# Optimization experiments

Measured on AMD Instinct MI355X. Metric: run time of the kernel, lower is better.

The kernel has to match this reference:

```python
import jax, jax.numpy as jnp
import numpy as np
import math

B, S, D, H, FF, L, V = 4, 2048, 512, 8, 2048, 4, 256
WINDOW, STRIDE, NGLOBAL = 256, 128, 16  # sparse pattern: causal & (local | strided | global)


def setup_inputs() -> dict:
    key = jax.random.key(0)
    ks = jax.random.split(key, 12)
    g = lambda k, shp: jax.random.normal(k, shp, dtype=jnp.float32) * 0.02
    return {
        "src_tokens": jax.random.randint(ks[0], (B, S), 0, V, dtype=jnp.int32),
        "emb": g(ks[1], (V, D)),
        "b_out": jnp.zeros((V,), jnp.float32),
        "Wq": g(ks[2], (L, D, D)), "bq": jnp.zeros((L, D), jnp.float32),
        "Wk": g(ks[3], (L, D, D)), "bk": jnp.zeros((L, D), jnp.float32),
        "Wv": g(ks[4], (L, D, D)), "bv": jnp.zeros((L, D), jnp.float32),
        "Wo": g(ks[5], (L, D, D)), "bo": jnp.zeros((L, D), jnp.float32),
        "ln1_g": jnp.ones((L, D), jnp.float32), "ln1_b": jnp.zeros((L, D), jnp.float32),
        "W1": g(ks[6], (L, D, FF)), "b1": jnp.zeros((L, FF), jnp.float32),
        "W2": g(ks[7], (L, FF, D)), "b2": jnp.zeros((L, D), jnp.float32),
        "ln2_g": jnp.ones((L, D), jnp.float32), "ln2_b": jnp.zeros((L, D), jnp.float32),
    }


def _pos_enc(seq_len, d_model):
    pos = jnp.arange(seq_len, dtype=jnp.float32)[:, None]
    div = jnp.exp(jnp.arange(0, d_model, 2, dtype=jnp.float32) * (-math.log(10000.0) / d_model))
    pe = jnp.zeros((seq_len, d_model), jnp.float32)
    pe = pe.at[:, 0::2].set(jnp.sin(pos * div)).at[:, 1::2].set(jnp.cos(pos * div))
    return pe


def _ln(x, g, b):
    m = x.mean(-1, keepdims=True)
    v = ((x - m) ** 2).mean(-1, keepdims=True)
    return (x - m) * jax.lax.rsqrt(v + 1e-5) * g + b


def _sparse_mask(seq_len):
    i = jnp.arange(seq_len)[:, None]
    j = jnp.arange(seq_len)[None, :]
    causal = j <= i
    local = (i - j) < WINDOW
    strided = ((i - j) % STRIDE) == 0
    glob = j < NGLOBAL
    return causal & (local | strided | glob)  # [S, S] bool


def reference(src_tokens, emb, b_out, Wq, bq, Wk, bk, Wv, bv, Wo, bo,
              ln1_g, ln1_b, W1, b1, W2, b2, ln2_g, ln2_b):
    dh = D // H
    x = emb[src_tokens] * math.sqrt(D) + _pos_enc(S, D)  # [B,S,D] (dropout inactive at eval)
    mask = _sparse_mask(S)
    for l in range(L):
        q = (x @ Wq[l] + bq[l]).reshape(B, S, H, dh)
        k = (x @ Wk[l] + bk[l]).reshape(B, S, H, dh)
        v = (x @ Wv[l] + bv[l]).reshape(B, S, H, dh)
        scores = jnp.einsum('bihd,bjhd->bhij', q, k) / math.sqrt(dh)
        scores = jnp.where(mask, scores, jnp.float32(-1e9))
        attn = jax.nn.softmax(scores, axis=-1)
        o = jnp.einsum('bhij,bjhd->bihd', attn, v).reshape(B, S, D)
        x = _ln(x + o @ Wo[l] + bo[l], ln1_g[l], ln1_b[l])      # post-LN residual
        h = jax.nn.relu(x @ W1[l] + b1[l])
        x = _ln(x + h @ W2[l] + b2[l], ln2_g[l], ln2_b[l])
    return x @ emb.T + b_out  # tied output projection -> [B,S,V]
```

## Files before the change

### kernel.cpp

```cpp
#include <hip/hip_runtime.h>
#include <hip/hip_bf16.h>
#include <math.h>

#define B_  4
#define S_  2048
#define D_  512
#define H_  8
#define DH_ 64
#define FF_ 2048
#define L_  4
#define V_  256
#define NTOK (B_ * S_)
#define XN  ((size_t)NTOK * D_)

typedef __attribute__((ext_vector_type(8))) short bf16x8;
typedef __attribute__((ext_vector_type(4))) float f32x4;
typedef __attribute__((ext_vector_type(8))) unsigned short u16x8;
typedef __attribute__((ext_vector_type(4))) unsigned short u16x4;

typedef const __attribute__((address_space(1))) unsigned int* gptr_u32;
typedef __attribute__((address_space(3))) unsigned int* lptr_u32;

__device__ __forceinline__ float bf2f(unsigned short u) {
    return __uint_as_float((unsigned)u << 16);
}
__device__ __forceinline__ unsigned short f2bf_bits(float f) {
    __hip_bfloat16 t = __float2bfloat16(f);
    return *(unsigned short*)&t;
}

__global__ void pe_table_kernel(float* __restrict__ PE) {
    int s = blockIdx.x;
    int d = threadIdx.x * 2;
    float ang = (float)s * expf((float)d * (-logf(10000.0f) / (float)D_));
    PE[(size_t)s * D_ + d]     = sinf(ang);
    PE[(size_t)s * D_ + d + 1] = cosf(ang);
}

__global__ void embed_kernel(const int* __restrict__ tok,
                             const float* __restrict__ emb,
                             const float* __restrict__ PE,
                             float* __restrict__ X,
                             __hip_bfloat16* __restrict__ Xb) {
    int bs = blockIdx.x;
    int s = bs % S_;
    int t = tok[bs];
    const float scale = 22.62741699796952f;
    int d = threadIdx.x * 4;
    float4 e = *(const float4*)(emb + (size_t)t * D_ + d);
    float4 p = *(const float4*)(PE + (size_t)s * D_ + d);
    float4 v = make_float4(e.x * scale + p.x, e.y * scale + p.y,
                           e.z * scale + p.z, e.w * scale + p.w);
    *(float4*)(X + (size_t)bs * D_ + d) = v;
    u16x4 pk = { f2bf_bits(v.x), f2bf_bits(v.y), f2bf_bits(v.z), f2bf_bits(v.w) };
    *(u16x4*)((unsigned short*)Xb + (size_t)bs * D_ + d) = pk;
}

__global__ void transpose_conv_kernel(const float* __restrict__ W,
                                      __hip_bfloat16* __restrict__ Wt,
                                      int K, int N) {
    const float* Wl = W + (size_t)blockIdx.z * K * N;
    __hip_bfloat16* Wtl = Wt + (size_t)blockIdx.z * K * N;
    __shared__ float t[32][33];
    int k0 = blockIdx.y * 32, n0 = blockIdx.x * 32;
    int tx = threadIdx.x & 31, ty = threadIdx.x >> 5;
    #pragma unroll
    for (int q = 0; q < 4; ++q)
        t[ty + q * 8][tx] = Wl[(size_t)(k0 + ty + q * 8) * N + n0 + tx];
    __syncthreads();
    #pragma unroll
    for (int q = 0; q < 4; ++q)
        Wtl[(size_t)(n0 + ty + q * 8) * K + k0 + tx] =
            __float2bfloat16(t[tx][ty + q * 8]);
}

__global__ void transpose_qkv_kernel(const float* __restrict__ Wq,
                                     const float* __restrict__ Wk,
                                     const float* __restrict__ Wv,
                                     __hip_bfloat16* __restrict__ dst) {
    int z = blockIdx.z, l = z / 3, which = z % 3;
    const float* src = (which == 0 ? Wq : which == 1 ? Wk : Wv) + (size_t)l * D_ * D_;
    __hip_bfloat16* d = dst + (size_t)l * 1536 * D_ + (size_t)which * D_ * D_;
    __shared__ float t[32][33];
    int k0 = blockIdx.y * 32, n0 = blockIdx.x * 32;
    int tx = threadIdx.x & 31, ty = threadIdx.x >> 5;
    #pragma unroll
    for (int q = 0; q < 4; ++q)
        t[ty + q * 8][tx] = src[(size_t)(k0 + ty + q * 8) * D_ + n0 + tx];
    __syncthreads();
    #pragma unroll
    for (int q = 0; q < 4; ++q)
        d[(size_t)(n0 + ty + q * 8) * D_ + k0 + tx] =
            __float2bfloat16(t[tx][ty + q * 8]);
}

__global__ void conv_bf16_kernel(const float* __restrict__ in,
                                 __hip_bfloat16* __restrict__ out, int n) {
    int i = blockIdx.x * 256 + threadIdx.x;
    if (i < n) out[i] = __float2bfloat16(in[i]);
}

template <int BM, int RELU, int OUT_MODE>
__global__ __launch_bounds__(256)
void gemm_bf16_kernel(const __hip_bfloat16* __restrict__ A,
                      const __hip_bfloat16* __restrict__ Bt,
                      const float* __restrict__ bias0,
                      const float* __restrict__ bias1,
                      const float* __restrict__ bias2,
                      float* __restrict__ Cf,
                      __hip_bfloat16* __restrict__ Cb0,
                      __hip_bfloat16* __restrict__ Cb1,
                      __hip_bfloat16* __restrict__ Cb2,
                      __hip_bfloat16* __restrict__ CbT,
                      int M, int N, int K) {
    constexpr int MI = BM / 32;
    __shared__ unsigned short As[2][BM * 32];
    __shared__ unsigned short Bs[2][128 * 32];
    int tid = threadIdx.x;
    int lane = tid & 63, wid = tid >> 6;
    int wm = (wid >> 1) * (BM / 2), wn = (wid & 1) * 64;
    int g = lane >> 4, il = lane & 15;

    int gx = gridDim.x;
    int fid = blockIdx.x + gx * blockIdx.y;
    int cpx = (gx * gridDim.y) >> 3;
    int swz = (fid & 7) * cpx + (fid >> 3);
    int m0 = (swz / gx) * BM, n0 = (swz % gx) * 128;

    auto stage = [&](int buf, int k0) {
        #pragma unroll
        for (int q = 0; q < BM / 64; ++q) {
            int idx = q * 256 + tid;
            int r = idx >> 2, c = idx & 3;
            int csw = (c ^ r) & 3;
            const __hip_bfloat16* sa = A + (size_t)(m0 + r) * K + k0 + csw * 8;
            __builtin_amdgcn_global_load_lds((gptr_u32)(const void*)sa,
                                             (lptr_u32)(void*)&As[buf][idx * 8], 16, 0, 0);
        }
        #pragma unroll
        for (int q = 0; q < 2; ++q) {
            int idx = q * 256 + tid;
            int r = idx >> 2, c = idx & 3;
            int csw = (c ^ r) & 3;
            const __hip_bfloat16* sb = Bt + (size_t)(n0 + r) * K + k0 + csw * 8;
            __builtin_amdgcn_global_load_lds((gptr_u32)(const void*)sb,
                                             (lptr_u32)(void*)&Bs[buf][idx * 8], 16, 0, 0);
        }
    };

    f32x4 acc[MI][4] = {};
    int NT = K >> 5;
    stage(0, 0);

    for (int t = 0; t < NT; ++t) {
        int cur = t & 1;
        if (t + 1 < NT) {
            stage(cur ^ 1, (t + 1) << 5);
            if constexpr (BM == 128)
                asm volatile("s_waitcnt vmcnt(4)" ::: "memory");
            else
                asm volatile("s_waitcnt vmcnt(3)" ::: "memory");
        } else {
            asm volatile("s_waitcnt vmcnt(0)" ::: "memory");
        }
        __builtin_amdgcn_s_barrier();

        bf16x8 af[MI], bf[4];
        #pragma unroll
        for (int i = 0; i < MI; ++i) {
            int m = wm + i * 16 + il;
            af[i] = *(const bf16x8*)&As[cur][m * 32 + ((g ^ m) & 3) * 8];
        }
        #pragma unroll
        for (int j = 0; j < 4; ++j) {
            int n = wn + j * 16 + il;
            bf[j] = *(const bf16x8*)&Bs[cur][n * 32 + ((g ^ n) & 3) * 8];
        }
        #pragma unroll
        for (int i = 0; i < MI; ++i)
            #pragma unroll
            for (int j = 0; j < 4; ++j)
                acc[i][j] = __builtin_amdgcn_mfma_f32_16x16x32_bf16(
                    af[i], bf[j], acc[i][j], 0, 0, 0);

        __builtin_amdgcn_s_barrier();
    }

    if constexpr (OUT_MODE == 4) {
        int seg = n0 >> 9;
        const float* bias = seg == 0 ? bias0 : seg == 1 ? bias1 : bias2;
        __hip_bfloat16* Crow = seg == 0 ? Cb0 : seg == 1 ? Cb1 : Cb2;
        int nseg = n0 & 511;
        #pragma unroll
        for (int j = 0; j < 4; ++j) {
            int coll = nseg + wn + j * 16 + il;
            float bv = bias[coll];
            #pragma unroll
            for (int i = 0; i < MI; ++i) {
                int row0 = m0 + wm + i * 16 + g * 4;
                if (seg < 2) {
                    #pragma unroll
                    for (int r = 0; r < 4; ++r)
                        Crow[(size_t)(row0 + r) * 512 + coll] =
                            __float2bfloat16(acc[i][j][r] + bv);
                } else {
                    u16x4 pk;
                    #pragma unroll
                    for (int r = 0; r < 4; ++r) {
                        float v = acc[i][j][r] + bv;
                        Crow[(size_t)(row0 + r) * 512 + coll] = __float2bfloat16(v);
                        pk[r] = f2bf_bits(v);
                    }
                    int hh = coll >> 6, dh = coll & 63;
                    int bb = row0 >> 11, s0 = row0 & 2047;
                    *(u16x4*)(CbT + ((size_t)((bb * 8 + hh) * 64 + dh) * 2048 + s0)) = pk;
                }
            }
        }
    } else {
        #pragma unroll
        for (int j = 0; j < 4; ++j) {
            int col = n0 + wn + j * 16 + il;
            float bv = bias0[col];
            #pragma unroll
            for (int i = 0; i < MI; ++i) {
                #pragma unroll
                for (int r = 0; r < 4; ++r) {
                    int row = m0 + wm + i * 16 + g * 4 + r;
                    float v = acc[i][j][r] + bv;
                    if (RELU) v = fmaxf(v, 0.0f);
                    if (OUT_MODE == 1) Cb0[(size_t)row * N + col] = __float2bfloat16(v);
                    else               Cf[(size_t)row * N + col] = v;
                }
            }
        }
    }
}

__device__ __forceinline__ bf16x8 lds_frag(const unsigned short* base, int row, int chunk) {
    int byte = (row << 7) + (((chunk ^ (row & 7)) & 7) << 4);
    return *(const bf16x8*)((const char*)base + byte);
}

__global__ __launch_bounds__(256)
void attn_mfma_kernel(const __hip_bfloat16* __restrict__ Q,
                      const __hip_bfloat16* __restrict__ K,
                      const __hip_bfloat16* __restrict__ V,
                      const __hip_bfloat16* __restrict__ VT,
                      __hip_bfloat16* __restrict__ O) {
    __shared__ unsigned short Ks[2][64 * 64];
    __shared__ unsigned short Vs[2][64 * 64];
    __shared__ unsigned short Ps[4][16 * 64];

    int fid = blockIdx.x + 32 * (blockIdx.y + 8 * blockIdx.z);
    int swz = (fid & 7) * 128 + (fid >> 3);
    int i0 = (swz & 31) * 64;
    int h  = (swz >> 5) & 7;
    int b  = swz >> 8;

    int tid = threadIdx.x, lane = tid & 63, wv = tid >> 6;
    int g = lane >> 4, il = lane & 15, g4 = g * 4;

    int nloc = min(i0 >> 6, 4) + 1;
    int add0 = (i0 > 256);
    int nt = nloc + add0;

    const size_t vt_off = (size_t)((b * 8 + h) * 64) * 2048;
    auto j0_of = [&](int t) { return (t < nloc) ? (i0 - 64 * t) : 0; };

    auto stage = [&](int buf, int j0) {
        #pragma unroll
        for (int q = 0; q < 2; ++q) {
            int idx = q * 256 + tid;
            int row = idx >> 3, c = idx & 7;
            int csw = c ^ (row & 7);
            const __hip_bfloat16* sk = K + (size_t)(b * 2048 + j0 + row) * 512 + h * 64 + csw * 8;
            __builtin_amdgcn_global_load_lds((gptr_u32)(const void*)sk,
                                             (lptr_u32)(void*)&Ks[buf][idx * 8], 16, 0, 0);
            const __hip_bfloat16* sv = VT + vt_off + (size_t)row * 2048 + j0 + csw * 8;
            __builtin_amdgcn_global_load_lds((gptr_u32)(const void*)sv,
                                             (lptr_u32)(void*)&Vs[buf][idx * 8], 16, 0, 0);
        }
    };

    int iq = i0 + wv * 16 + il;
    bf16x8 qf[2];
    #pragma unroll
    for (int kh = 0; kh < 2; ++kh)
        qf[kh] = *(const bf16x8*)(Q + (size_t)(b * 2048 + iq) * 512 + h * 64 + kh * 32 + g * 8);

    stage(0, j0_of(0));

    float qfl[16];
    #pragma unroll
    for (int kh = 0; kh < 2; ++kh)
        #pragma unroll
        for (int e = 0; e < 8; ++e)
            qfl[kh * 8 + e] = bf2f(((u16x8)qf[kh])[e]);

    unsigned short* myP = Ps[wv];
    f32x4 o[4] = {};
    float os[16] = {};
    float m = -1e30f, l = 0.0f;
    const float CSC = 0.18033688011112042f;

    const unsigned short* Kbase = (const unsigned short*)(K + (size_t)b * 2048 * 512 + h * 64);
    const unsigned short* Vbase = (const unsigned short*)(V + (size_t)b * 2048 * 512 + h * 64);
    for (int j = iq - 384; j >= 16; j -= 128) {
        const unsigned short* kr = Kbase + (size_t)j * 512;
        u16x8 k0 = *(const u16x8*)(kr + g * 8);
        u16x8 k1 = *(const u16x8*)(kr + 32 + g * 8);
        float dot = 0.0f;
        #pragma unroll
        for (int e = 0; e < 8; ++e)
            dot += qfl[e] * bf2f(k0[e]) + qfl[8 + e] * bf2f(k1[e]);
        dot += __shfl_xor(dot, 16);
        dot += __shfl_xor(dot, 32);
        float s2 = dot * CSC;
        float mn = fmaxf(m, s2);
        float al = exp2f(m - mn);
        float p = exp2f(s2 - mn);
        l = l * al + p;
        m = mn;
        const unsigned short* vr = Vbase + (size_t)j * 512;
        u16x8 v0 = *(const u16x8*)(vr + g * 8);
        u16x8 v1 = *(const u16x8*)(vr + 32 + g * 8);
        #pragma unroll
        for (int e = 0; e < 8; ++e) {
            os[e]     = os[e]     * al + p * bf2f(v0[e]);
            os[8 + e] = os[8 + e] * al + p * bf2f(v1[e]);
        }
    }

    for (int t = 0; t < nt; ++t) {
        __syncthreads();
        int cur = t & 1;
        if (t + 1 < nt) stage(cur ^ 1, j0_of(t + 1));
        int j0 = j0_of(t);
        bool gtile = (t >= nloc);
        bool dtile = (t == 0);

        f32x4 s[4] = {};
        __builtin_amdgcn_s_setprio(1);
        if (gtile) {
            #pragma unroll
            for (int kh = 0; kh < 2; ++kh) {
                bf16x8 a = lds_frag(Ks[cur], il, kh * 4 + g);
                s[0] = __builtin_amdgcn_mfma_f32_16x16x32_bf16(a, qf[kh], s[0], 0, 0, 0);
            }
        } else if (dtile) {
            #pragma unroll
            for (int kh = 0; kh < 2; ++kh)
                #pragma unroll
                for (int jn = 0; jn < 4; ++jn)
                    if (jn <= wv) {
                        bf16x8 a = lds_frag(Ks[cur], jn * 16 + il, kh * 4 + g);
                        s[jn] = __builtin_amdgcn_mfma_f32_16x16x32_bf16(a, qf[kh], s[jn], 0, 0, 0);
                    }
        } else {
            #pragma unroll
            for (int kh = 0; kh < 2; ++kh)
                #pragma unroll
                for (int jn = 0; jn < 4; ++jn) {
                    bf16x8 a = lds_frag(Ks[cur], jn * 16 + il, kh * 4 + g);
                    s[jn] = __builtin_amdgcn_mfma_f32_16x16x32_bf16(a, qf[kh], s[jn], 0, 0, 0);
                }
        }
        __builtin_amdgcn_s_setprio(0);

        float mloc = -1e30f;
        if (gtile) {
            #pragma unroll
            for (int r = 0; r < 4; ++r) {
                float sv = s[0][r] * CSC;
                s[0][r] = sv;
                mloc = fmaxf(mloc, sv);
            }
        } else if (dtile) {
            #pragma unroll
            for (int jn = 0; jn < 4; ++jn) {
                if (jn < wv) {
                    #pragma unroll
                    for (int r = 0; r < 4; ++r) {
                        float sv = s[jn][r] * CSC;
                        s[jn][r] = sv;
                        mloc = fmaxf(mloc, sv);
                    }
                } else if (jn == wv) {
                    #pragma unroll
                    for (int r = 0; r < 4; ++r) {
                        float sv = (g4 + r <= il) ? s[jn][r] * CSC : -1e30f;
                        s[jn][r] = sv;
                        mloc = fmaxf(mloc, sv);
                    }
                }
            }
        } else if (t == 4) {
            #pragma unroll
            for (int jn = 0; jn < 4; ++jn)
                #pragma unroll
                for (int r = 0; r < 4; ++r) {
                    int jg = j0 + jn * 16 + g4 + r;
                    int dij = iq - jg;
                    bool ok = (dij < 256) || ((dij & 127) == 0) || (jg < 16);
                    float sv = ok ? s[jn][r] * CSC : -1e30f;
                    s[jn][r] = sv;
                    mloc = fmaxf(mloc, sv);
                }
        } else {
            #pragma unroll
            for (int jn = 0; jn < 4; ++jn)
                #pragma unroll
                for (int r = 0; r < 4; ++r) {
                    float sv = s[jn][r] * CSC;
                    s[jn][r] = sv;
                    mloc = fmaxf(mloc, sv);
                }
        }
        mloc = fmaxf(mloc, __shfl_xor(mloc, 16));
        mloc = fmaxf(mloc, __shfl_xor(mloc, 32));
        float mn = fmaxf(m, mloc);
        float al = exp2f(m - mn);

        float lloc = 0.0f;
        if (gtile) {
            #pragma unroll
            for (int r = 0; r < 4; ++r) {
                float p = exp2f(s[0][r] - mn);
                s[0][r] = p;
                lloc += p;
            }
        } else {
            #pragma unroll
            for (int jn = 0; jn < 4; ++jn) {
                if (dtile && jn > wv) continue;
                #pragma unroll
                for (int r = 0; r < 4; ++r) {
                    float p = exp2f(s[jn][r] - mn);
                    s[jn][r] = p;
                    lloc += p;
                }
            }
        }
        lloc += __shfl_xor(lloc, 16);
        lloc += __shfl_xor(lloc, 32);
        l = l * al + lloc;
        m = mn;

        if (!__all(al == 1.0f)) {
            float ar[4];
            #pragma unroll
            for (int r = 0; r < 4; ++r) ar[r] = __shfl(al, g4 + r);
            #pragma unroll
            for (int dn = 0; dn < 4; ++dn)
                #pragma unroll
                for (int r = 0; r < 4; ++r) o[dn][r] *= ar[r];
            #pragma unroll
            for (int e = 0; e < 16; ++e) os[e] *= al;
        }

        #pragma unroll
        for (int jn = 0; jn < 4; ++jn) {
            if (gtile && jn >= 2) continue;
            u16x4 pk = { 0, 0, 0, 0 };
            bool live = gtile ? (jn == 0) : (!dtile || jn <= wv);
            if (live) {
                #pragma unroll
                for (int r = 0; r < 4; ++r) pk[r] = f2bf_bits(s[jn][r]);
            }
            int byte = ((il << 7) + (jn << 5) + (g << 3)) ^ ((il & 7) << 4);
            *(u16x4*)((char*)myP + byte) = pk;
        }
        int khmax = (gtile || (dtile && wv < 2)) ? 1 : 2;
        __builtin_amdgcn_s_setprio(1);
        #pragma unroll
        for (int kh = 0; kh < 2; ++kh) {
            if (kh < khmax) {
                bf16x8 pa = lds_frag(myP, il, kh * 4 + g);
                #pragma unroll
                for (int dn = 0; dn < 4; ++dn) {
                    bf16x8 bv = lds_frag(Vs[cur], dn * 16 + il, kh * 4 + g);
                    o[dn] = __builtin_amdgcn_mfma_f32_16x16x32_bf16(pa, bv, o[dn], 0, 0, 0);
                }
            }
        }
        __builtin_amdgcn_s_setprio(0);
    }

    __syncthreads();
    float* osl = (float*)&Ks[0][0] + wv * 1024;
    #pragma unroll
    for (int kh = 0; kh < 2; ++kh)
        #pragma unroll
        for (int e = 0; e < 8; ++e)
            osl[il * 64 + kh * 32 + g * 8 + e] = os[kh * 8 + e];
    __syncthreads();

    float li[4];
    #pragma unroll
    for (int r = 0; r < 4; ++r) li[r] = 1.0f / __shfl(l, g4 + r);
    #pragma unroll
    for (int dn = 0; dn < 4; ++dn)
        #pragma unroll
        for (int r = 0; r < 4; ++r) {
            int row = i0 + wv * 16 + g4 + r;
            float add = osl[(g4 + r) * 64 + dn * 16 + il];
            O[(size_t)(b * 2048 + row) * 512 + h * 64 + dn * 16 + il] =
                __float2bfloat16((o[dn][r] + add) * li[r]);
        }
}

__global__ __launch_bounds__(256)
void add_ln_kernel(float* __restrict__ X,
                   const __hip_bfloat16* __restrict__ T,
                   const float* __restrict__ g,
                   const float* __restrict__ bb,
                   __hip_bfloat16* __restrict__ Xb) {
    size_t row = blockIdx.x * 4 + (threadIdx.x >> 6);
    int lane = threadIdx.x & 63;
    int d0 = lane * 8;
    float4 x0 = *(const float4*)(X + row * D_ + d0);
    float4 x1 = *(const float4*)(X + row * D_ + d0 + 4);
    u16x8 tv = *(const u16x8*)((const unsigned short*)T + row * D_ + d0);
    float v[8] = { x0.x + bf2f(tv[0]), x0.y + bf2f(tv[1]),
                   x0.z + bf2f(tv[2]), x0.w + bf2f(tv[3]),
                   x1.x + bf2f(tv[4]), x1.y + bf2f(tv[5]),
                   x1.z + bf2f(tv[6]), x1.w + bf2f(tv[7]) };
    float sum = 0.0f;
    #pragma unroll
    for (int q = 0; q < 8; ++q) sum += v[q];
    #pragma unroll
    for (int o = 32; o; o >>= 1) sum += __shfl_xor(sum, o);
    float mean = sum * (1.0f / D_);
    float var = 0.0f;
    #pragma unroll
    for (int q = 0; q < 8; ++q) { float dd = v[q] - mean; var += dd * dd; }
    #pragma unroll
    for (int o = 32; o; o >>= 1) var += __shfl_xor(var, o);
    var *= (1.0f / D_);
    float r = rsqrtf(var + 1e-5f);
    float4 g0 = *(const float4*)(g + d0),  g1 = *(const float4*)(g + d0 + 4);
    float4 b0 = *(const float4*)(bb + d0), b1 = *(const float4*)(bb + d0 + 4);
    float y[8];
    y[0] = (v[0]-mean)*r*g0.x+b0.x; y[1] = (v[1]-mean)*r*g0.y+b0.y;
    y[2] = (v[2]-mean)*r*g0.z+b0.z; y[3] = (v[3]-mean)*r*g0.w+b0.w;
    y[4] = (v[4]-mean)*r*g1.x+b1.x; y[5] = (v[5]-mean)*r*g1.y+b1.y;
    y[6] = (v[6]-mean)*r*g1.z+b1.z; y[7] = (v[7]-mean)*r*g1.w+b1.w;
    *(float4*)(X + row * D_ + d0)     = make_float4(y[0], y[1], y[2], y[3]);
    *(float4*)(X + row * D_ + d0 + 4) = make_float4(y[4], y[5], y[6], y[7]);
    u16x8 pk;
    #pragma unroll
    for (int q = 0; q < 8; ++q) pk[q] = f2bf_bits(y[q]);
    *(u16x8*)((unsigned short*)Xb + row * D_ + d0) = pk;
}

extern "C" void kernel_launch(void* const* d_in, const int* in_sizes, int n_in,
                              void* d_out, int out_size, void* d_ws, size_t ws_size,
                              hipStream_t stream) {
    const int*   tok   = (const int*)  d_in[0];
    const float* emb   = (const float*)d_in[1];
    const float* b_out = (const float*)d_in[2];
    const float* Wq    = (const float*)d_in[3];
    const float* bq    = (const float*)d_in[4];
    const float* Wk    = (const float*)d_in[5];
    const float* bk    = (const float*)d_in[6];
    const float* Wv    = (const float*)d_in[7];
    const float* bv    = (const float*)d_in[8];
    const float* Wo    = (const float*)d_in[9];
    const float* bo    = (const float*)d_in[10];
    const float* ln1g  = (const float*)d_in[11];
    const float* ln1b  = (const float*)d_in[12];
    const float* W1    = (const float*)d_in[13];
    const float* b1    = (const float*)d_in[14];
    const float* W2    = (const float*)d_in[15];
    const float* b2    = (const float*)d_in[16];
    const float* ln2g  = (const float*)d_in[17];
    const float* ln2b  = (const float*)d_in[18];
    float* out = (float*)d_out;

    char* w = (char*)d_ws;
    auto alloc = [&](size_t bytes) {
        char* p = w;
        w += (bytes + 255) & ~(size_t)255;
        return p;
    };
    float*          X   = (float*)         alloc(XN * 4);
    __hip_bfloat16* Xb  = (__hip_bfloat16*)alloc(XN * 2);
    __hip_bfloat16* Tb  = (__hip_bfloat16*)alloc(XN * 2);
    char* uni = alloc(XN * 2 * 5);
    __hip_bfloat16* Qb  = (__hip_bfloat16*)uni;
    __hip_bfloat16* Kb  = Qb + XN;
    __hip_bfloat16* Vb  = Kb + XN;
    __hip_bfloat16* VTb = Vb + XN;
    __hip_bfloat16* Ob  = VTb + XN;
    __hip_bfloat16* Hb  = (__hip_bfloat16*)uni;
    __hip_bfloat16* Wqkvt = (__hip_bfloat16*)alloc((size_t)L_ * 1536 * D_ * 2);
    __hip_bfloat16* Wot  = (__hip_bfloat16*)alloc((size_t)L_ * D_ * D_ * 2);
    __hip_bfloat16* W1t  = (__hip_bfloat16*)alloc((size_t)L_ * D_ * FF_ * 2);
    __hip_bfloat16* W2t  = (__hip_bfloat16*)alloc((size_t)L_ * FF_ * D_ * 2);
    __hip_bfloat16* embb = (__hip_bfloat16*)alloc((size_t)V_ * D_ * 2);
    float*          PE   = (float*)alloc((size_t)S_ * D_ * 4);

    {
        pe_table_kernel<<<S_, 256, 0, stream>>>(PE);
        dim3 gqkv(D_ / 32, D_ / 32, L_ * 3);
        transpose_qkv_kernel<<<gqkv, 256, 0, stream>>>(Wq, Wk, Wv, Wqkvt);
        dim3 gdd(D_ / 32, D_ / 32, L_);
        transpose_conv_kernel<<<gdd, 256, 0, stream>>>(Wo, Wot, D_, D_);
        dim3 g1(FF_ / 32, D_ / 32, L_);
        transpose_conv_kernel<<<g1, 256, 0, stream>>>(W1, W1t, D_, FF_);
        dim3 g2(D_ / 32, FF_ / 32, L_);
        transpose_conv_kernel<<<g2, 256, 0, stream>>>(W2, W2t, FF_, D_);
        conv_bf16_kernel<<<(V_ * D_ + 255) / 256, 256, 0, stream>>>(emb, embb, V_ * D_);
    }

    embed_kernel<<<NTOK, 128, 0, stream>>>(tok, emb, PE, X, Xb);

    dim3 blk(256);
    dim3 gqkv(1536 / 128, NTOK / 128);
    dim3 g512n(D_ / 128, NTOK / 64);
    dim3 gff (FF_ / 128, NTOK / 128);
    dim3 gout(V_ / 128, NTOK / 64);
    dim3 gattn(S_ / 64, H_, B_);
    dim3 gln(NTOK / 4);

    for (int l = 0; l < L_; ++l) {
        const __hip_bfloat16* wqkv = Wqkvt + (size_t)l * 1536 * D_;
        const __hip_bfloat16* wot = Wot + (size_t)l * D_ * D_;
        const __hip_bfloat16* w1t = W1t + (size_t)l * D_ * FF_;
        const __hip_bfloat16* w2t = W2t + (size_t)l * FF_ * D_;

        gemm_bf16_kernel<128, 0, 4><<<gqkv, blk, 0, stream>>>(
            Xb, wqkv, bq + l * D_, bk + l * D_, bv + l * D_,
            nullptr, Qb, Kb, Vb, VTb, NTOK, 1536, D_);

        attn_mfma_kernel<<<gattn, blk, 0, stream>>>(Qb, Kb, Vb, VTb, Ob);

        gemm_bf16_kernel<64, 0, 1><<<g512n, blk, 0, stream>>>(
            Ob, wot, bo + l * D_, nullptr, nullptr,
            nullptr, Tb, nullptr, nullptr, nullptr, NTOK, D_, D_);
        add_ln_kernel<<<gln, blk, 0, stream>>>(X, Tb, ln1g + l * D_, ln1b + l * D_, Xb);

        gemm_bf16_kernel<128, 1, 1><<<gff, blk, 0, stream>>>(
            Xb, w1t, b1 + l * FF_, nullptr, nullptr,
            nullptr, Hb, nullptr, nullptr, nullptr, NTOK, FF_, D_);
        gemm_bf16_kernel<64, 0, 1><<<g512n, blk, 0, stream>>>(
            Hb, w2t, b2 + l * D_, nullptr, nullptr,
            nullptr, Tb, nullptr, nullptr, nullptr, NTOK, D_, FF_);
        add_ln_kernel<<<gln, blk, 0, stream>>>(X, Tb, ln2g + l * D_, ln2b + l * D_, Xb);
    }

    gemm_bf16_kernel<64, 0, 0><<<gout, blk, 0, stream>>>(
        Xb, embb, b_out, nullptr, nullptr,
        out, nullptr, nullptr, nullptr, nullptr, NTOK, V_, D_);
}
```

Before: 692.5 us.

## Pair complementary query tiles per attention block and batch strided-key softmax

```diff
diff --git a/kernel.cpp b/kernel.cpp
--- a/kernel.cpp
+++ b/kernel.cpp
@@ -252,21 +252,20 @@
     __shared__ unsigned short Vs[2][64 * 64];
     __shared__ unsigned short Ps[4][16 * 64];
 
-    int fid = blockIdx.x + 32 * (blockIdx.y + 8 * blockIdx.z);
-    int swz = (fid & 7) * 128 + (fid >> 3);
-    int i0 = (swz & 31) * 64;
-    int h  = (swz >> 5) & 7;
-    int b  = swz >> 8;
+    int d = blockIdx.x + 16 * (blockIdx.y + 8 * blockIdx.z);
+    int xcd = d & 7, t8 = d >> 3;
+    int qtr = t8 & 15, gsub = t8 >> 4;
+    int qt = ((qtr & 1) << 3) | ((qtr & 2) << 1) | ((qtr & 4) >> 1) | ((qtr & 8) >> 3);
+    int grp = xcd * 4 + gsub;
+    int h = grp & 7, b = grp >> 3;
 
     int tid = threadIdx.x, lane = tid & 63, wv = tid >> 6;
     int g = lane >> 4, il = lane & 15, g4 = g * 4;
 
-    int nloc = min(i0 >> 6, 4) + 1;
-    int add0 = (i0 > 256);
-    int nt = nloc + add0;
-
     const size_t vt_off = (size_t)((b * 8 + h) * 64) * 2048;
-    auto j0_of = [&](int t) { return (t < nloc) ? (i0 - 64 * t) : 0; };
+    const unsigned short* Kbase = (const unsigned short*)(K + (size_t)b * 2048 * 512 + h * 64);
+    const unsigned short* Vbase = (const unsigned short*)(V + (size_t)b * 2048 * 512 + h * 64);
+    const float CSC = 0.18033688011112042f;
 
     auto stage = [&](int buf, int j0) {
         #pragma unroll
@@ -283,231 +282,257 @@
         }
     };
 
-    int iq = i0 + wv * 16 + il;
-    bf16x8 qf[2];
-    #pragma unroll
-    for (int kh = 0; kh < 2; ++kh)
-        qf[kh] = *(const bf16x8*)(Q + (size_t)(b * 2048 + iq) * 512 + h * 64 + kh * 32 + g * 8);
-
-    stage(0, j0_of(0));
-
-    float qfl[16];
-    #pragma unroll
-    for (int kh = 0; kh < 2; ++kh)
-        #pragma unroll
-        for (int e = 0; e < 8; ++e)
-            qfl[kh * 8 + e] = bf2f(((u16x8)qf[kh])[e]);
-
     unsigned short* myP = Ps[wv];
-    f32x4 o[4] = {};
-    float os[16] = {};
-    float m = -1e30f, l = 0.0f;
-    const float CSC = 0.18033688011112042f;
-
-    const unsigned short* Kbase = (const unsigned short*)(K + (size_t)b * 2048 * 512 + h * 64);
-    const unsigned short* Vbase = (const unsigned short*)(V + (size_t)b * 2048 * 512 + h * 64);
-    for (int j = iq - 384; j >= 16; j -= 128) {
-        const unsigned short* kr = Kbase + (size_t)j * 512;
-        u16x8 k0 = *(const u16x8*)(kr + g * 8);
-        u16x8 k1 = *(const u16x8*)(kr + 32 + g * 8);
-        float dot = 0.0f;
-        #pragma unroll
-        for (int e = 0; e < 8; ++e)
-            dot += qfl[e] * bf2f(k0[e]) + qfl[8 + e] * bf2f(k1[e]);
-        dot += __shfl_xor(dot, 16);
-        dot += __shfl_xor(dot, 32);
-        float s2 = dot * CSC;
-        float mn = fmaxf(m, s2);
-        float al = exp2f(m - mn);
-        float p = exp2f(s2 - mn);
-        l = l * al + p;
-        m = mn;
-        const unsigned short* vr = Vbase + (size_t)j * 512;
-        u16x8 v0 = *(const u16x8*)(vr + g * 8);
-        u16x8 v1 = *(const u16x8*)(vr + 32 + g * 8);
-        #pragma unroll
-        for (int e = 0; e < 8; ++e) {
-            os[e]     = os[e]     * al + p * bf2f(v0[e]);
-            os[8 + e] = os[8 + e] * al + p * bf2f(v1[e]);
-        }
-    }
-
-    for (int t = 0; t < nt; ++t) {
+
+    #pragma unroll 1
+    for (int half = 0; half < 2; ++half) {
+        int i0 = (half == 0) ? qt * 64 : (31 - qt) * 64;
+        int nloc = min(i0 >> 6, 4) + 1;
+        int add0 = (i0 > 256);
+        int nt = nloc + add0;
+        auto j0_of = [&](int t) { return (t < nloc) ? (i0 - 64 * t) : 0; };
+
         __syncthreads();
-        int cur = t & 1;
-        if (t + 1 < nt) stage(cur ^ 1, j0_of(t + 1));
-        int j0 = j0_of(t);
-        bool gtile = (t >= nloc);
-        bool dtile = (t == 0);
-
-        f32x4 s[4] = {};
-        __builtin_amdgcn_s_setprio(1);
-        if (gtile) {
-            #pragma unroll
-            for (int kh = 0; kh < 2; ++kh) {
-                bf16x8 a = lds_frag(Ks[cur], il, kh * 4 + g);
-                s[0] = __builtin_amdgcn_mfma_f32_16x16x32_bf16(a, qf[kh], s[0], 0, 0, 0);
-            }
-        } else if (dtile) {
-            #pragma unroll
-            for (int kh = 0; kh < 2; ++kh)
-                #pragma unroll
-                for (int jn = 0; jn < 4; ++jn)
-                    if (jn <= wv) {
+        stage(0, i0);
+
+        int iq = i0 + wv * 16 + il;
+        bf16x8 qf[2];
+        #pragma unroll
+        for (int kh = 0; kh < 2; ++kh)
+            qf[kh] = *(const bf16x8*)(Q + (size_t)(b * 2048 + iq) * 512 + h * 64 + kh * 32 + g * 8);
+        float qfl[16];
+        #pragma unroll
+        for (int kh = 0; kh < 2; ++kh)
+            #pragma unroll
+            for (int e = 0; e < 8; ++e)
+                qfl[kh * 8 + e] = bf2f(((u16x8)qf[kh])[e]);
+
+        f32x4 o[4] = {};
+        float os[16] = {};
+        float m = -1e30f, l = 0.0f;
+
+        int nst = (iq >= 400) ? ((iq - 400) >> 7) + 1 : 0;
+        if (nst > 0) {
+            float sarr[13];
+            #pragma unroll
+            for (int mm = 0; mm < 13; ++mm) {
+                int j = iq - 384 - 128 * mm;
+                int jc = (j >= 16) ? j : 16;
+                const unsigned short* kr = Kbase + (size_t)jc * 512;
+                u16x8 k0 = *(const u16x8*)(kr + g * 8);
+                u16x8 k1 = *(const u16x8*)(kr + 32 + g * 8);
+                float dot = 0.0f;
+                #pragma unroll
+                for (int e = 0; e < 8; ++e)
+                    dot += qfl[e] * bf2f(k0[e]) + qfl[8 + e] * bf2f(k1[e]);
+                dot += __shfl_xor(dot, 16);
+                dot += __shfl_xor(dot, 32);
+                sarr[mm] = (j >= 16) ? dot * CSC : -1e30f;
+            }
+            float mmax = -1e30f;
+            #pragma unroll
+            for (int mm = 0; mm < 13; ++mm) mmax = fmaxf(mmax, sarr[mm]);
+            float p[13];
+            float lsum = 0.0f;
+            #pragma unroll
+            for (int mm = 0; mm < 13; ++mm) {
+                p[mm] = exp2f(sarr[mm] - mmax);
+                lsum += p[mm];
+            }
+            #pragma unroll
+            for (int mm = 0; mm < 13; ++mm) {
+                int j = iq - 384 - 128 * mm;
+                int jc = (j >= 16) ? j : 16;
+                const unsigned short* vr = Vbase + (size_t)jc * 512;
+                u16x8 v0 = *(const u16x8*)(vr + g * 8);
+                u16x8 v1 = *(const u16x8*)(vr + 32 + g * 8);
+                #pragma unroll
+                for (int e = 0; e < 8; ++e) {
+                    os[e]     += p[mm] * bf2f(v0[e]);
+                    os[8 + e] += p[mm] * bf2f(v1[e]);
+                }
+            }
+            m = mmax;
+            l = lsum;
+        }
+
+        for (int t = 0; t < nt; ++t) {
+            __syncthreads();
+            int cur = t & 1;
+            if (t + 1 < nt) stage(cur ^ 1, j0_of(t + 1));
+            int j0 = j0_of(t);
+            bool gtile = (t >= nloc);
+            bool dtile = (t == 0);
+
+            f32x4 s[4] = {};
+            __builtin_amdgcn_s_setprio(1);
+            if (gtile) {
+                #pragma unroll
+                for (int kh = 0; kh < 2; ++kh) {
+                    bf16x8 a = lds_frag(Ks[cur], il, kh * 4 + g);
+                    s[0] = __builtin_amdgcn_mfma_f32_16x16x32_bf16(a, qf[kh], s[0], 0, 0, 0);
+                }
+            } else if (dtile) {
+                #pragma unroll
+                for (int kh = 0; kh < 2; ++kh)
+                    #pragma unroll
+                    for (int jn = 0; jn < 4; ++jn)
+                        if (jn <= wv) {
+                            bf16x8 a = lds_frag(Ks[cur], jn * 16 + il, kh * 4 + g);
+                            s[jn] = __builtin_amdgcn_mfma_f32_16x16x32_bf16(a, qf[kh], s[jn], 0, 0, 0);
+                        }
+            } else {
+                #pragma unroll
+                for (int kh = 0; kh < 2; ++kh)
+                    #pragma unroll
+                    for (int jn = 0; jn < 4; ++jn) {
                         bf16x8 a = lds_frag(Ks[cur], jn * 16 + il, kh * 4 + g);
                         s[jn] = __builtin_amdgcn_mfma_f32_16x16x32_bf16(a, qf[kh], s[jn], 0, 0, 0);
                     }
-        } else {
-            #pragma unroll
-            for (int kh = 0; kh < 2; ++kh)
+            }
+            __builtin_amdgcn_s_setprio(0);
+
+            float mloc = -1e30f;
+            if (gtile) {
+                #pragma unroll
+                for (int r = 0; r < 4; ++r) {
+                    float sv = s[0][r] * CSC;
+                    s[0][r] = sv;
+                    mloc = fmaxf(mloc, sv);
+                }
+            } else if (dtile) {
                 #pragma unroll
                 for (int jn = 0; jn < 4; ++jn) {
-                    bf16x8 a = lds_frag(Ks[cur], jn * 16 + il, kh * 4 + g);
-                    s[jn] = __builtin_amdgcn_mfma_f32_16x16x32_bf16(a, qf[kh], s[jn], 0, 0, 0);
-                }
-        }
-        __builtin_amdgcn_s_setprio(0);
-
-        float mloc = -1e30f;
-        if (gtile) {
-            #pragma unroll
-            for (int r = 0; r < 4; ++r) {
-                float sv = s[0][r] * CSC;
-                s[0][r] = sv;
-                mloc = fmaxf(mloc, sv);
-            }
-        } else if (dtile) {
-            #pragma unroll
-            for (int jn = 0; jn < 4; ++jn) {
-                if (jn < wv) {
+                    if (jn < wv) {
+                        #pragma unroll
+                        for (int r = 0; r < 4; ++r) {
+                            float sv = s[jn][r] * CSC;
+                            s[jn][r] = sv;
+                            mloc = fmaxf(mloc, sv);
+                        }
+                    } else if (jn == wv) {
+                        #pragma unroll
+                        for (int r = 0; r < 4; ++r) {
+                            float sv = (g4 + r <= il) ? s[jn][r] * CSC : -1e30f;
+                            s[jn][r] = sv;
+                            mloc = fmaxf(mloc, sv);
+                        }
+                    }
+                }
+            } else if (t == 4) {
+                #pragma unroll
+                for (int jn = 0; jn < 4; ++jn)
+                    #pragma unroll
+                    for (int r = 0; r < 4; ++r) {
+                        int jg = j0 + jn * 16 + g4 + r;
+                        int dij = iq - jg;
+                        bool ok = (dij < 256) || ((dij & 127) == 0) || (jg < 16);
+                        float sv = ok ? s[jn][r] * CSC : -1e30f;
+                        s[jn][r] = sv;
+                        mloc = fmaxf(mloc, sv);
+                    }
+            } else {
+                #pragma unroll
+                for (int jn = 0; jn < 4; ++jn)
                     #pragma unroll
                     for (int r = 0; r < 4; ++r) {
                         float sv = s[jn][r] * CSC;
                         s[jn][r] = sv;
                         mloc = fmaxf(mloc, sv);
                     }
-                } else if (jn == wv) {
+            }
+            mloc = fmaxf(mloc, __shfl_xor(mloc, 16));
+            mloc = fmaxf(mloc, __shfl_xor(mloc, 32));
+            float mn = fmaxf(m, mloc);
+            float al = exp2f(m - mn);
+
+            float lloc = 0.0f;
+            if (gtile) {
+                #pragma unroll
+                for (int r = 0; r < 4; ++r) {
+                    float p = exp2f(s[0][r] - mn);
+                    s[0][r] = p;
+                    lloc += p;
+                }
+            } else {
+                #pragma unroll
+                for (int jn = 0; jn < 4; ++jn) {
+                    if (dtile && jn > wv) continue;
                     #pragma unroll
                     for (int r = 0; r < 4; ++r) {
-                        float sv = (g4 + r <= il) ? s[jn][r] * CSC : -1e30f;
-                        s[jn][r] = sv;
-                        mloc = fmaxf(mloc, sv);
+                        float p = exp2f(s[jn][r] - mn);
+                        s[jn][r] = p;
+                        lloc += p;
                     }
                 }
             }
-        } else if (t == 4) {
-            #pragma unroll
-            for (int jn = 0; jn < 4; ++jn)
-                #pragma unroll
-                for (int r = 0; r < 4; ++r) {
-                    int jg = j0 + jn * 16 + g4 + r;
-                    int dij = iq - jg;
-                    bool ok = (dij < 256) || ((dij & 127) == 0) || (jg < 16);
-                    float sv = ok ? s[jn][r] * CSC : -1e30f;
-                    s[jn][r] = sv;
-                    mloc = fmaxf(mloc, sv);
-                }
-        } else {
-            #pragma unroll
-            for (int jn = 0; jn < 4; ++jn)
-                #pragma unroll
-                for (int r = 0; r < 4; ++r) {
-                    float sv = s[jn][r] * CSC;
-                    s[jn][r] = sv;
-                    mloc = fmaxf(mloc, sv);
-                }
-        }
-        mloc = fmaxf(mloc, __shfl_xor(mloc, 16));
-        mloc = fmaxf(mloc, __shfl_xor(mloc, 32));
-        float mn = fmaxf(m, mloc);
-        float al = exp2f(m - mn);
-
-        float lloc = 0.0f;
-        if (gtile) {
+            lloc += __shfl_xor(lloc, 16);
+            lloc += __shfl_xor(lloc, 32);
+            l = l * al + lloc;
+            m = mn;
+
+            if (!__all(al == 1.0f)) {
+                float ar[4];
+                #pragma unroll
+                for (int r = 0; r < 4; ++r) ar[r] = __shfl(al, g4 + r);
+                #pragma unroll
+                for (int dn = 0; dn < 4; ++dn)
+                    #pragma unroll
+                    for (int r = 0; r < 4; ++r) o[dn][r] *= ar[r];
+                #pragma unroll
+                for (int e = 0; e < 16; ++e) os[e] *= al;
+            }
+
+            #pragma unroll
+            for (int jn = 0; jn < 4; ++jn) {
+                if (gtile && jn >= 2) continue;
+                u16x4 pk = { 0, 0, 0, 0 };
+                bool live = gtile ? (jn == 0) : (!dtile || jn <= wv);
+                if (live) {
+                    #pragma unroll
+                    for (int r = 0; r < 4; ++r) pk[r] = f2bf_bits(s[jn][r]);
+                }
+                int byte = ((il << 7) + (jn << 5) + (g << 3)) ^ ((il & 7) << 4);
+                *(u16x4*)((char*)myP + byte) = pk;
+            }
+            int khmax = (gtile || (dtile && wv < 2)) ? 1 : 2;
+            __builtin_amdgcn_s_setprio(1);
+            #pragma unroll
+            for (int kh = 0; kh < 2; ++kh) {
+                if (kh < khmax) {
+                    bf16x8 pa = lds_frag(myP, il, kh * 4 + g);
+                    #pragma unroll
+                    for (int dn = 0; dn < 4; ++dn) {
+                        bf16x8 bv = lds_frag(Vs[cur], dn * 16 + il, kh * 4 + g);
+                        o[dn] = __builtin_amdgcn_mfma_f32_16x16x32_bf16(pa, bv, o[dn], 0, 0, 0);
+                    }
+                }
+            }
+            __builtin_amdgcn_s_setprio(0);
+        }
+
+        __syncthreads();
+        float* osl = (float*)&Ks[0][0] + wv * 1024;
+        #pragma unroll
+        for (int kh = 0; kh < 2; ++kh)
+            #pragma unroll
+            for (int e = 0; e < 8; ++e)
+                osl[il * 64 + kh * 32 + g * 8 + e] = os[kh * 8 + e];
+        __syncthreads();
+
+        float li[4];
+        #pragma unroll
+        for (int r = 0; r < 4; ++r) li[r] = 1.0f / __shfl(l, g4 + r);
+        #pragma unroll
+        for (int dn = 0; dn < 4; ++dn)
             #pragma unroll
             for (int r = 0; r < 4; ++r) {
-                float p = exp2f(s[0][r] - mn);
-                s[0][r] = p;
-                lloc += p;
-            }
-        } else {
-            #pragma unroll
-            for (int jn = 0; jn < 4; ++jn) {
-                if (dtile && jn > wv) continue;
-                #pragma unroll
-                for (int r = 0; r < 4; ++r) {
-                    float p = exp2f(s[jn][r] - mn);
-                    s[jn][r] = p;
-                    lloc += p;
-                }
-            }
-        }
-        lloc += __shfl_xor(lloc, 16);
-        lloc += __shfl_xor(lloc, 32);
-        l = l * al + lloc;
-        m = mn;
-
-        if (!__all(al == 1.0f)) {
-            float ar[4];
-            #pragma unroll
-            for (int r = 0; r < 4; ++r) ar[r] = __shfl(al, g4 + r);
-            #pragma unroll
-            for (int dn = 0; dn < 4; ++dn)
-                #pragma unroll
-                for (int r = 0; r < 4; ++r) o[dn][r] *= ar[r];
-            #pragma unroll
-            for (int e = 0; e < 16; ++e) os[e] *= al;
-        }
-
-        #pragma unroll
-        for (int jn = 0; jn < 4; ++jn) {
-            if (gtile && jn >= 2) continue;
-            u16x4 pk = { 0, 0, 0, 0 };
-            bool live = gtile ? (jn == 0) : (!dtile || jn <= wv);
-            if (live) {
-                #pragma unroll
-                for (int r = 0; r < 4; ++r) pk[r] = f2bf_bits(s[jn][r]);
-            }
-            int byte = ((il << 7) + (jn << 5) + (g << 3)) ^ ((il & 7) << 4);
-            *(u16x4*)((char*)myP + byte) = pk;
-        }
-        int khmax = (gtile || (dtile && wv < 2)) ? 1 : 2;
-        __builtin_amdgcn_s_setprio(1);
-        #pragma unroll
-        for (int kh = 0; kh < 2; ++kh) {
-            if (kh < khmax) {
-                bf16x8 pa = lds_frag(myP, il, kh * 4 + g);
-                #pragma unroll
-                for (int dn = 0; dn < 4; ++dn) {
-                    bf16x8 bv = lds_frag(Vs[cur], dn * 16 + il, kh * 4 + g);
-                    o[dn] = __builtin_amdgcn_mfma_f32_16x16x32_bf16(pa, bv, o[dn], 0, 0, 0);
-                }
-            }
-        }
-        __builtin_amdgcn_s_setprio(0);
+                int row = i0 + wv * 16 + g4 + r;
+                float add = osl[(g4 + r) * 64 + dn * 16 + il];
+                O[(size_t)(b * 2048 + row) * 512 + h * 64 + dn * 16 + il] =
+                    __float2bfloat16((o[dn][r] + add) * li[r]);
+            }
     }
-
-    __syncthreads();
-    float* osl = (float*)&Ks[0][0] + wv * 1024;
-    #pragma unroll
-    for (int kh = 0; kh < 2; ++kh)
-        #pragma unroll
-        for (int e = 0; e < 8; ++e)
-            osl[il * 64 + kh * 32 + g * 8 + e] = os[kh * 8 + e];
-    __syncthreads();
-
-    float li[4];
-    #pragma unroll
-    for (int r = 0; r < 4; ++r) li[r] = 1.0f / __shfl(l, g4 + r);
-    #pragma unroll
-    for (int dn = 0; dn < 4; ++dn)
-        #pragma unroll
-        for (int r = 0; r < 4; ++r) {
-            int row = i0 + wv * 16 + g4 + r;
-            float add = osl[(g4 + r) * 64 + dn * 16 + il];
-            O[(size_t)(b * 2048 + row) * 512 + h * 64 + dn * 16 + il] =
-                __float2bfloat16((o[dn][r] + add) * li[r]);
-        }
 }
 
 __global__ __launch_bounds__(256)
@@ -621,7 +646,7 @@
     dim3 g512n(D_ / 128, NTOK / 64);
     dim3 gff (FF_ / 128, NTOK / 128);
     dim3 gout(V_ / 128, NTOK / 64);
-    dim3 gattn(S_ / 64, H_, B_);
+    dim3 gattn(S_ / 128, H_, B_);
     dim3 gln(NTOK / 4);
 
     for (int l = 0; l < L_; ++l) {
```

Result: slower. 754.6 us (+9.0%).
